# Optimization experiments

Measured on AMD Instinct MI355X. Metric: run time of the kernel, lower is better.

## Reference

```python
import jax, jax.numpy as jnp
import numpy as np

BATCH, INPUT_SIZE, STEPS = 256, 512, 256
HIDDEN = 512


def setup_inputs() -> dict:
    key = jax.random.key(0)
    ks = jax.random.split(key, 5)
    s = 1.0 / np.sqrt(HIDDEN)
    return {
        "x": jax.random.normal(ks[0], (BATCH, INPUT_SIZE, STEPS), dtype=jnp.float32),
        "weight_ih": jax.random.uniform(ks[1], (3 * HIDDEN, INPUT_SIZE), jnp.float32, -s, s),
        "weight_hh": jax.random.uniform(ks[2], (3 * HIDDEN, HIDDEN), jnp.float32, -s, s),
        "bias_ih": jax.random.uniform(ks[3], (3 * HIDDEN,), jnp.float32, -s, s),
        "bias_hh": jax.random.uniform(ks[4], (3 * HIDDEN,), jnp.float32, -s, s),
    }


def reference(x, weight_ih, weight_hh, bias_ih, bias_hh):
    # x: [B, input_size, steps]; run a GRUCell over the time axis, return final hidden.
    B = x.shape[0]
    # Precompute all input projections in one big GEMM: [steps, B, 3H]
    gi_all = jnp.einsum('bis,gi->sbg', x, weight_ih) + bias_ih

    def step(h, gi):
        gh = h @ weight_hh.T + bias_hh  # [B, 3H]
        i_r, i_z, i_n = jnp.split(gi, 3, axis=-1)
        h_r, h_z, h_n = jnp.split(gh, 3, axis=-1)
        r = jax.nn.sigmoid(i_r + h_r)
        z = jax.nn.sigmoid(i_z + h_z)
        n = jnp.tanh(i_n + r * h_n)
        h_new = (1.0 - z) * n + z * h
        return h_new, None

    h0 = jnp.zeros((B, HIDDEN), dtype=x.dtype)
    h_final, _ = jax.lax.scan(step, h0, gi_all)
    return h_final
```

## Files before the change

### kernel.cpp

```cpp
#include <hip/hip_runtime.h>
#include <stdint.h>

typedef __attribute__((ext_vector_type(8))) short bf16x8;
typedef __attribute__((ext_vector_type(4))) short s16x4;
typedef __attribute__((ext_vector_type(4))) float f32x4;

#define AS1 __attribute__((address_space(1)))
#define AS3 __attribute__((address_space(3)))

static __device__ __forceinline__ void gload_lds16(const void* g, void* l) {
  __builtin_amdgcn_global_load_lds((const AS1 unsigned int*)g,
                                   (AS3 unsigned int*)l, 16, 0, 0);
}

static __device__ __forceinline__ short f2bs(float f) {
  unsigned u = __builtin_bit_cast(unsigned, f);
  unsigned r = (u + 0x7fffu + ((u >> 16) & 1u)) >> 16;
  return (short)r;
}
static __device__ __forceinline__ float bs2f(short s) {
  unsigned u = ((unsigned)(unsigned short)s) << 16;
  return __builtin_bit_cast(float, u);
}

static __device__ __forceinline__ float sigmoid_f(float x) {
  return 1.0f / (1.0f + __expf(-x));
}
static __device__ __forceinline__ float tanh_f(float x) {
  float ax = fabsf(x);
  float e  = __expf(-2.0f * ax);
  float t  = (1.0f - e) / (1.0f + e);
  return copysignf(t, x);
}

#define BATCH 256
#define HID   512
#define STEPS 256
#define G3    1536

__global__ __launch_bounds__(256) void convert_kernel(const float* __restrict__ src,
                                                      short* __restrict__ dst, int n4) {
  int i = blockIdx.x * 256 + threadIdx.x;
  if (i < n4) {
    float4 v = *(const float4*)(src + (size_t)i * 4);
    s16x4 o;
    o[0] = f2bs(v.x); o[1] = f2bs(v.y); o[2] = f2bs(v.z); o[3] = f2bs(v.w);
    *(s16x4*)(dst + (size_t)i * 4) = o;
  }
}

__global__ __launch_bounds__(256) void transpose_kernel(const float* __restrict__ x,
                                                        short* __restrict__ xT) {
  int bx = blockIdx.x;
  int st = bx & 7, it = (bx >> 3) & 15, b = bx >> 7;
  int s0 = st * 32, i0 = it * 32;
  int tid = threadIdx.x;
  __shared__ float tile[32][33];
  int il = tid >> 3, s4 = (tid & 7) * 4;
  float4 v = *(const float4*)(x + (size_t)b * 131072 + (size_t)(i0 + il) * 256 + s0 + s4);
  tile[il][s4 + 0] = v.x; tile[il][s4 + 1] = v.y;
  tile[il][s4 + 2] = v.z; tile[il][s4 + 3] = v.w;
  __syncthreads();
  int sl = tid >> 3, iv = (tid & 7) * 4;
  s16x4 o;
  o[0] = f2bs(tile[iv + 0][sl]); o[1] = f2bs(tile[iv + 1][sl]);
  o[2] = f2bs(tile[iv + 2][sl]); o[3] = f2bs(tile[iv + 3][sl]);
  *(s16x4*)(xT + (size_t)(s0 + sl) * 131072 + (size_t)b * 512 + i0 + iv) = o;
}

__global__ __launch_bounds__(256) void phase1_kernel(const short* __restrict__ A,
                                                     const short* __restrict__ B,
                                                     const float* __restrict__ bias,
                                                     short* __restrict__ out, int M) {
  int MT = M >> 7;
  int bx = blockIdx.x;
  int mt = bx % MT, nt = bx / MT;
  int m0 = mt * 128, n0 = nt * 128;
  int tid = threadIdx.x, w = tid >> 6, lane = tid & 63;
  int lm = lane & 15, q = lane >> 4;
  int wm = w & 1, wn = w >> 1;
  __shared__ short As[128 * 32];
  __shared__ short Bs[128 * 32];
  f32x4 acc[4][4] = {};
  int srow = lane >> 2;
  int scol = (lane & 3) * 8;

  for (int kt = 0; kt < 16; ++kt) {
#pragma unroll
    for (int i2 = 0; i2 < 2; ++i2) {
      int i = w * 2 + i2;
      int row = i * 16 + srow;
      gload_lds16(A + (size_t)(m0 + row) * 512 + kt * 32 + scol, As + i * 512);
      gload_lds16(B + (size_t)(n0 + row) * 512 + kt * 32 + scol, Bs + i * 512);
    }
    __syncthreads();
    bf16x8 av[4], bv[4];
#pragma unroll
    for (int f = 0; f < 4; ++f) {
      av[f] = *(const bf16x8*)(As + (wm * 64 + f * 16 + lm) * 32 + q * 8);
      bv[f] = *(const bf16x8*)(Bs + (wn * 64 + f * 16 + lm) * 32 + q * 8);
    }
#pragma unroll
    for (int fm = 0; fm < 4; ++fm)
#pragma unroll
      for (int fn = 0; fn < 4; ++fn)
        acc[fm][fn] = __builtin_amdgcn_mfma_f32_16x16x32_bf16(av[fm], bv[fn], acc[fm][fn], 0, 0, 0);
    __syncthreads();
  }
#pragma unroll
  for (int fn = 0; fn < 4; ++fn) {
    int g = n0 + wn * 64 + fn * 16 + lm;
    float bi = bias[g];
#pragma unroll
    for (int fm = 0; fm < 4; ++fm) {
      int rb = m0 + wm * 64 + fm * 16 + q * 4;
#pragma unroll
      for (int r = 0; r < 4; ++r)
        out[(size_t)(rb + r) * G3 + g] = f2bs(acc[fm][fn][r] + bi);
    }
  }
}

__global__ __launch_bounds__(256) void scan_kernel(const short* __restrict__ gi,
                                                   const short* __restrict__ Whh,
                                                   const float* __restrict__ bias_hh,
                                                   short* __restrict__ hbuf,
                                                   unsigned* __restrict__ counters,
                                                   float* __restrict__ hmaster,
                                                   int CH, int step_base, int first) {
  int bid = blockIdx.x;
  int xcd = bid & 7, slot = bid >> 3;
  int group = xcd + 8 * (slot >> 4);
  int j = slot & 15;
  int tid = threadIdx.x;
  int w = tid >> 6, lane = tid & 63;
  int lm = lane & 15, q = lane >> 4;
  int grow = group * 16;

  __shared__ short h_lds[16 * 520];
  __shared__ float gh_lds[16][100];
  __shared__ float h_loc[512];
  __shared__ float bhh[96];

  bf16x8 Bf[2][16];
  if (w < 3) {
#pragma unroll
    for (int tau = 0; tau < 2; ++tau)
#pragma unroll
      for (int kt = 0; kt < 16; ++kt) {
        int row = w * 512 + j * 32 + tau * 16 + lm;
        Bf[tau][kt] = *(const bf16x8*)(Whh + (size_t)row * 512 + kt * 32 + q * 8);
      }
  }

  if (tid < 96) {
    int p = tid >> 5, cc = tid & 31;
    bhh[tid] = bias_hh[p * 512 + j * 32 + cc];
  }
#pragma unroll
  for (int u = 0; u < 2; ++u) {
    int idx = tid + u * 256;
    int r = idx >> 5, cc = idx & 31;
    h_loc[idx] = first ? 0.0f : hmaster[(size_t)(grow + r) * 512 + j * 32 + cc];
  }
  __syncthreads();

  int i0 = tid, i1 = tid + 256;
  const short* gp0 = gi + (size_t)(grow + (i0 >> 5)) * G3 + j * 32 + (i0 & 31);
  const short* gp1 = gi + (size_t)(grow + (i1 >> 5)) * G3 + j * 32 + (i1 & 31);
  const size_t gstride = (size_t)256 * G3;

  short pg0r = gp0[0], pg0z = gp0[512], pg0n = gp0[1024];
  short pg1r = gp1[0], pg1z = gp1[512], pg1n = gp1[1024];

  for (int t = 0; t < CH; ++t) {
    int gstep = step_base + t;
    int p = gstep & 1;
    const short* hsrc = hbuf + (size_t)p * (256 * 512) + (size_t)grow * 512;
    const short* pa = hsrc + (size_t)(tid >> 6) * 512 + (size_t)(tid & 63) * 8;

    bf16x8 t0, t1, t2, t3;
    asm volatile(
        "global_load_dwordx4 %0, %4, off sc0 sc1\n\t"
        "global_load_dwordx4 %1, %5, off sc0 sc1\n\t"
        "global_load_dwordx4 %2, %6, off sc0 sc1\n\t"
        "global_load_dwordx4 %3, %7, off sc0 sc1\n\t"
        "s_waitcnt vmcnt(0)"
        : "=&v"(t0), "=&v"(t1), "=&v"(t2), "=&v"(t3)
        : "v"(pa), "v"(pa + 2048), "v"(pa + 4096), "v"(pa + 6144)
        : "memory");

    float cg0r = bs2f(pg0r), cg0z = bs2f(pg0z), cg0n = bs2f(pg0n);
    float cg1r = bs2f(pg1r), cg1z = bs2f(pg1z), cg1n = bs2f(pg1n);
    {
      size_t o = (size_t)((t + 1 < CH) ? (t + 1) : t) * gstride;
      pg0r = gp0[o]; pg0z = gp0[o + 512]; pg0n = gp0[o + 1024];
      pg1r = gp1[o]; pg1z = gp1[o + 512]; pg1n = gp1[o + 1024];
    }

    short* ld = h_lds + (tid >> 6) * 520 + (tid & 63) * 8;
    *(bf16x8*)(ld)            = t0;
    *(bf16x8*)(ld + 4 * 520)  = t1;
    *(bf16x8*)(ld + 8 * 520)  = t2;
    *(bf16x8*)(ld + 12 * 520) = t3;
    __syncthreads();

    if (w < 3) {
      f32x4 a0 = {0.f,0.f,0.f,0.f}, a1 = {0.f,0.f,0.f,0.f};
      f32x4 a2 = {0.f,0.f,0.f,0.f}, a3 = {0.f,0.f,0.f,0.f};
#pragma unroll
      for (int kt = 0; kt < 8; ++kt) {
        bf16x8 a = *(const bf16x8*)(h_lds + lm * 520 + kt * 32 + q * 8);
        a0 = __builtin_amdgcn_mfma_f32_16x16x32_bf16(a, Bf[0][kt], a0, 0, 0, 0);
        a1 = __builtin_amdgcn_mfma_f32_16x16x32_bf16(a, Bf[1][kt], a1, 0, 0, 0);
      }
#pragma unroll
      for (int kt = 8; kt < 16; ++kt) {
        bf16x8 a = *(const bf16x8*)(h_lds + lm * 520 + kt * 32 + q * 8);
        a2 = __builtin_amdgcn_mfma_f32_16x16x32_bf16(a, Bf[0][kt], a2, 0, 0, 0);
        a3 = __builtin_amdgcn_mfma_f32_16x16x32_bf16(a, Bf[1][kt], a3, 0, 0, 0);
      }
#pragma unroll
      for (int r = 0; r < 4; ++r) {
        gh_lds[q * 4 + r][w * 32 + lm]      = a0[r] + a2[r];
        gh_lds[q * 4 + r][w * 32 + 16 + lm] = a1[r] + a3[r];
      }
    }
    __syncthreads();

    {
      int r = i0 >> 5, cc = i0 & 31;
      float hr = gh_lds[r][cc]      + bhh[cc];
      float hz = gh_lds[r][32 + cc] + bhh[32 + cc];
      float hn = gh_lds[r][64 + cc] + bhh[64 + cc];
      float rr = sigmoid_f(cg0r + hr);
      float zz = sigmoid_f(cg0z + hz);
      float nn = tanh_f(cg0n + rr * hn);
      h_loc[i0] = (1.0f - zz) * nn + zz * h_loc[i0];
    }
    {
      int r = i1 >> 5, cc = i1 & 31;
      float hr = gh_lds[r][cc]      + bhh[cc];
      float hz = gh_lds[r][32 + cc] + bhh[32 + cc];
      float hn = gh_lds[r][64 + cc] + bhh[64 + cc];
      float rr = sigmoid_f(cg1r + hr);
      float zz = sigmoid_f(cg1z + hz);
      float nn = tanh_f(cg1n + rr * hn);
      h_loc[i1] = (1.0f - zz) * nn + zz * h_loc[i1];
    }
    __syncthreads();

    if (w == 0) {
      short* hdst = hbuf + (size_t)(1 - p) * (256 * 512)
                  + (size_t)(grow + (lane >> 2)) * 512 + j * 32 + (lane & 3) * 8;
      int base = (lane >> 2) * 32 + (lane & 3) * 8;
      bf16x8 hb;
#pragma unroll
      for (int e = 0; e < 8; ++e) hb[e] = f2bs(h_loc[base + e]);
      asm volatile("global_store_dwordx4 %0, %1, off sc0 sc1\n\ts_waitcnt vmcnt(0)"
                   :: "v"(hdst), "v"(hb) : "memory");
      if (lane == 0) {
        unsigned* cp = counters + (size_t)(group * 16 + j) * 16;
        unsigned val = (unsigned)(gstep + 1);
        asm volatile("global_store_dword %0, %1, off sc0 sc1" :: "v"(cp), "v"(val) : "memory");
      }
    } else if (w == 1) {
      if (t < CH - 1 && lane < 16) {
        const unsigned* cpl = counters + (size_t)(group * 16 + lane) * 16;
        unsigned tgt = (unsigned)(gstep + 1);
        unsigned v; int it = 0;
        do {
          asm volatile("global_load_dword %0, %1, off sc0 sc1\n\ts_waitcnt vmcnt(0)"
                       : "=v"(v) : "v"(cpl) : "memory");
          if (v >= tgt) break;
          __builtin_amdgcn_s_sleep(1);
        } while (++it < (1 << 20));
      }
    }
    __syncthreads();
  }

#pragma unroll
  for (int u = 0; u < 2; ++u) {
    int idx = tid + u * 256;
    int r = idx >> 5, cc = idx & 31;
    hmaster[(size_t)(grow + r) * 512 + j * 32 + cc] = h_loc[idx];
  }
}

extern "C" void kernel_launch(void* const* d_in, const int* in_sizes, int n_in,
                              void* d_out, int out_size, void* d_ws, size_t ws_size,
                              hipStream_t stream) {
  const float* x   = (const float*)d_in[0];
  const float* Wih = (const float*)d_in[1];
  const float* Whh = (const float*)d_in[2];
  const float* bih = (const float*)d_in[3];
  const float* bhh = (const float*)d_in[4];
  float* out = (float*)d_out;
  char* ws = (char*)d_ws;

  const size_t XT_BYTES   = (size_t)256 * 256 * 512 * 2;
  const size_t W_BYTES    = (size_t)1536 * 512 * 2;
  const size_t HBUF_BYTES = (size_t)2 * 256 * 512 * 2;
  const size_t CNT_BYTES  = 16384;
  const size_t FIXED = XT_BYTES + 2 * W_BYTES + HBUF_BYTES + CNT_BYTES + 4096;

  int CH = 256;
  while (CH > 4 && FIXED + (size_t)CH * 256 * G3 * 2 > ws_size) CH >>= 1;

  size_t off = 0;
  short* gi = (short*)(ws + off);          off += (size_t)CH * 256 * G3 * 2;
  short* xT = (short*)(ws + off);          off += XT_BYTES;
  short* WihB = (short*)(ws + off);        off += W_BYTES;
  short* WhhB = (short*)(ws + off);        off += W_BYTES;
  short* hbuf = (short*)(ws + off);        off += HBUF_BYTES;
  unsigned* counters = (unsigned*)(ws + off);

  hipMemsetAsync(hbuf, 0, HBUF_BYTES + CNT_BYTES, stream);

  convert_kernel<<<768, 256, 0, stream>>>(Wih, WihB, 196608);
  convert_kernel<<<768, 256, 0, stream>>>(Whh, WhhB, 196608);
  transpose_kernel<<<32768, 256, 0, stream>>>(x, xT);

  int nch = 256 / CH;
  for (int c = 0; c < nch; ++c) {
    int M = CH * 256;
    phase1_kernel<<<(M / 128) * 12, 256, 0, stream>>>(
        xT + (size_t)c * CH * 256 * 512, WihB, bih, gi, M);
    scan_kernel<<<256, 256, 0, stream>>>(gi, WhhB, bhh, hbuf, counters, out,
                                         CH, c * CH, c == 0 ? 1 : 0);
  }
}
```

Baseline: 1.079 ms.

## Replace counter-based cross-block barrier with step-tagged hidden-state words

Each hidden-state element is now stored as a 32-bit word holding the bf16 value in the high half and the step number in the low half. Consumers poll the hidden buffer until every tag matches the expected step, then strip the tags into LDS. This removes the separate counter store/poll phase and two block-wide barriers per step. In exchange the hidden-state traffic doubles, and readers re-fetch the whole tile while spinning.

```diff
diff --git a/kernel.cpp b/kernel.cpp
--- a/kernel.cpp
+++ b/kernel.cpp
@@ -4,6 +4,7 @@
 typedef __attribute__((ext_vector_type(8))) short bf16x8;
 typedef __attribute__((ext_vector_type(4))) short s16x4;
 typedef __attribute__((ext_vector_type(4))) float f32x4;
+typedef __attribute__((ext_vector_type(4))) unsigned u32x4;
 
 #define AS1 __attribute__((address_space(1)))
 #define AS3 __attribute__((address_space(3)))
@@ -124,8 +125,7 @@
 __global__ __launch_bounds__(256) void scan_kernel(const short* __restrict__ gi,
                                                    const short* __restrict__ Whh,
                                                    const float* __restrict__ bias_hh,
-                                                   short* __restrict__ hbuf,
-                                                   unsigned* __restrict__ counters,
+                                                   unsigned* __restrict__ hbuf,
                                                    float* __restrict__ hmaster,
                                                    int CH, int step_base, int first) {
   int bid = blockIdx.x;
@@ -173,22 +173,60 @@
   short pg0r = gp0[0], pg0z = gp0[512], pg0n = gp0[1024];
   short pg1r = gp1[0], pg1z = gp1[512], pg1n = gp1[1024];
 
+  unsigned o0 = (unsigned)tid * 16u;
+  const int r0 = tid >> 7;
+  const int colb = (tid & 127) * 4;
+  short* lp = h_lds + r0 * 520 + colb;
+  unsigned* grp_base = hbuf + (size_t)group * 8192;
+
   for (int t = 0; t < CH; ++t) {
     int gstep = step_base + t;
     int p = gstep & 1;
-    const short* hsrc = hbuf + (size_t)p * (256 * 512) + (size_t)grow * 512;
-    const short* pa = hsrc + (size_t)(tid >> 6) * 512 + (size_t)(tid & 63) * 8;
-
-    bf16x8 t0, t1, t2, t3;
-    asm volatile(
-        "global_load_dwordx4 %0, %4, off sc0 sc1\n\t"
-        "global_load_dwordx4 %1, %5, off sc0 sc1\n\t"
-        "global_load_dwordx4 %2, %6, off sc0 sc1\n\t"
-        "global_load_dwordx4 %3, %7, off sc0 sc1\n\t"
-        "s_waitcnt vmcnt(0)"
-        : "=&v"(t0), "=&v"(t1), "=&v"(t2), "=&v"(t3)
-        : "v"(pa), "v"(pa + 2048), "v"(pa + 4096), "v"(pa + 6144)
-        : "memory");
+    const unsigned* src = grp_base + (size_t)p * 131072;
+    unsigned want = (unsigned)gstep;
+
+    u32x4 v0, v1, v2, v3, v4, v5, v6, v7;
+    int spin = 0;
+    for (;;) {
+      asm volatile(
+          "global_load_dwordx4 %0, %8, %16 sc0 sc1\n\t"
+          "global_load_dwordx4 %1, %9, %16 sc0 sc1\n\t"
+          "global_load_dwordx4 %2, %10, %16 sc0 sc1\n\t"
+          "global_load_dwordx4 %3, %11, %16 sc0 sc1\n\t"
+          "global_load_dwordx4 %4, %12, %16 sc0 sc1\n\t"
+          "global_load_dwordx4 %5, %13, %16 sc0 sc1\n\t"
+          "global_load_dwordx4 %6, %14, %16 sc0 sc1\n\t"
+          "global_load_dwordx4 %7, %15, %16 sc0 sc1\n\t"
+          "s_waitcnt vmcnt(0)"
+          : "=&v"(v0), "=&v"(v1), "=&v"(v2), "=&v"(v3),
+            "=&v"(v4), "=&v"(v5), "=&v"(v6), "=&v"(v7)
+          : "v"(o0), "v"(o0 + 4096u), "v"(o0 + 8192u), "v"(o0 + 12288u),
+            "v"(o0 + 16384u), "v"(o0 + 20480u), "v"(o0 + 24576u), "v"(o0 + 28672u),
+            "s"(src)
+          : "memory");
+      unsigned d;
+      d  = (v0[0] ^ want) | (v0[1] ^ want) | (v0[2] ^ want) | (v0[3] ^ want);
+      d |= (v1[0] ^ want) | (v1[1] ^ want) | (v1[2] ^ want) | (v1[3] ^ want);
+      d |= (v2[0] ^ want) | (v2[1] ^ want) | (v2[2] ^ want) | (v2[3] ^ want);
+      d |= (v3[0] ^ want) | (v3[1] ^ want) | (v3[2] ^ want) | (v3[3] ^ want);
+      d |= (v4[0] ^ want) | (v4[1] ^ want) | (v4[2] ^ want) | (v4[3] ^ want);
+      d |= (v5[0] ^ want) | (v5[1] ^ want) | (v5[2] ^ want) | (v5[3] ^ want);
+      d |= (v6[0] ^ want) | (v6[1] ^ want) | (v6[2] ^ want) | (v6[3] ^ want);
+      d |= (v7[0] ^ want) | (v7[1] ^ want) | (v7[2] ^ want) | (v7[3] ^ want);
+      if (((d & 0xffffu) == 0u) || (++spin > (1 << 16))) break;
+      __builtin_amdgcn_s_sleep(1);
+    }
+
+#define STASH(vv, c)                                                         \
+    {                                                                        \
+      s16x4 o_;                                                              \
+      o_[0] = (short)(vv[0] >> 16); o_[1] = (short)(vv[1] >> 16);            \
+      o_[2] = (short)(vv[2] >> 16); o_[3] = (short)(vv[3] >> 16);            \
+      *(s16x4*)(lp + (c) * 1040) = o_;                                       \
+    }
+    STASH(v0, 0) STASH(v1, 1) STASH(v2, 2) STASH(v3, 3)
+    STASH(v4, 4) STASH(v5, 5) STASH(v6, 6) STASH(v7, 7)
+#undef STASH
 
     float cg0r = bs2f(pg0r), cg0z = bs2f(pg0z), cg0n = bs2f(pg0n);
     float cg1r = bs2f(pg1r), cg1z = bs2f(pg1z), cg1n = bs2f(pg1n);
@@ -197,12 +235,6 @@
       pg0r = gp0[o]; pg0z = gp0[o + 512]; pg0n = gp0[o + 1024];
       pg1r = gp1[o]; pg1z = gp1[o + 512]; pg1n = gp1[o + 1024];
     }
-
-    short* ld = h_lds + (tid >> 6) * 520 + (tid & 63) * 8;
-    *(bf16x8*)(ld)            = t0;
-    *(bf16x8*)(ld + 4 * 520)  = t1;
-    *(bf16x8*)(ld + 8 * 520)  = t2;
-    *(bf16x8*)(ld + 12 * 520) = t3;
     __syncthreads();
 
     if (w < 3) {
@@ -228,6 +260,8 @@
     }
     __syncthreads();
 
+    unsigned tagp = (unsigned)(gstep + 1);
+    unsigned* dstb = grp_base + (size_t)(1 - p) * 131072;
     {
       int r = i0 >> 5, cc = i0 & 31;
       float hr = gh_lds[r][cc]      + bhh[cc];
@@ -236,7 +270,11 @@
       float rr = sigmoid_f(cg0r + hr);
       float zz = sigmoid_f(cg0z + hz);
       float nn = tanh_f(cg0n + rr * hn);
-      h_loc[i0] = (1.0f - zz) * nn + zz * h_loc[i0];
+      float hv = (1.0f - zz) * nn + zz * h_loc[i0];
+      h_loc[i0] = hv;
+      unsigned val = (((unsigned)(unsigned short)f2bs(hv)) << 16) | tagp;
+      unsigned* dp = dstb + r * 512 + j * 32 + cc;
+      asm volatile("global_store_dword %0, %1, off sc0 sc1" :: "v"(dp), "v"(val) : "memory");
     }
     {
       int r = i1 >> 5, cc = i1 & 31;
@@ -246,38 +284,12 @@
       float rr = sigmoid_f(cg1r + hr);
       float zz = sigmoid_f(cg1z + hz);
       float nn = tanh_f(cg1n + rr * hn);
-      h_loc[i1] = (1.0f - zz) * nn + zz * h_loc[i1];
-    }
-    __syncthreads();
-
-    if (w == 0) {
-      short* hdst = hbuf + (size_t)(1 - p) * (256 * 512)
-                  + (size_t)(grow + (lane >> 2)) * 512 + j * 32 + (lane & 3) * 8;
-      int base = (lane >> 2) * 32 + (lane & 3) * 8;
-      bf16x8 hb;
-#pragma unroll
-      for (int e = 0; e < 8; ++e) hb[e] = f2bs(h_loc[base + e]);
-      asm volatile("global_store_dwordx4 %0, %1, off sc0 sc1\n\ts_waitcnt vmcnt(0)"
-                   :: "v"(hdst), "v"(hb) : "memory");
-      if (lane == 0) {
-        unsigned* cp = counters + (size_t)(group * 16 + j) * 16;
-        unsigned val = (unsigned)(gstep + 1);
-        asm volatile("global_store_dword %0, %1, off sc0 sc1" :: "v"(cp), "v"(val) : "memory");
-      }
-    } else if (w == 1) {
-      if (t < CH - 1 && lane < 16) {
-        const unsigned* cpl = counters + (size_t)(group * 16 + lane) * 16;
-        unsigned tgt = (unsigned)(gstep + 1);
-        unsigned v; int it = 0;
-        do {
-          asm volatile("global_load_dword %0, %1, off sc0 sc1\n\ts_waitcnt vmcnt(0)"
-                       : "=v"(v) : "v"(cpl) : "memory");
-          if (v >= tgt) break;
-          __builtin_amdgcn_s_sleep(1);
-        } while (++it < (1 << 20));
-      }
-    }
-    __syncthreads();
+      float hv = (1.0f - zz) * nn + zz * h_loc[i1];
+      h_loc[i1] = hv;
+      unsigned val = (((unsigned)(unsigned short)f2bs(hv)) << 16) | tagp;
+      unsigned* dp = dstb + r * 512 + j * 32 + cc;
+      asm volatile("global_store_dword %0, %1, off sc0 sc1" :: "v"(dp), "v"(val) : "memory");
+    }
   }
 
 #pragma unroll
@@ -301,9 +313,8 @@
 
   const size_t XT_BYTES   = (size_t)256 * 256 * 512 * 2;
   const size_t W_BYTES    = (size_t)1536 * 512 * 2;
-  const size_t HBUF_BYTES = (size_t)2 * 256 * 512 * 2;
-  const size_t CNT_BYTES  = 16384;
-  const size_t FIXED = XT_BYTES + 2 * W_BYTES + HBUF_BYTES + CNT_BYTES + 4096;
+  const size_t HBUF_BYTES = (size_t)2 * 256 * 512 * 4;
+  const size_t FIXED = XT_BYTES + 2 * W_BYTES + HBUF_BYTES + 4096;
 
   int CH = 256;
   while (CH > 4 && FIXED + (size_t)CH * 256 * G3 * 2 > ws_size) CH >>= 1;
@@ -313,10 +324,9 @@
   short* xT = (short*)(ws + off);          off += XT_BYTES;
   short* WihB = (short*)(ws + off);        off += W_BYTES;
   short* WhhB = (short*)(ws + off);        off += W_BYTES;
-  short* hbuf = (short*)(ws + off);        off += HBUF_BYTES;
-  unsigned* counters = (unsigned*)(ws + off);
-
-  hipMemsetAsync(hbuf, 0, HBUF_BYTES + CNT_BYTES, stream);
+  unsigned* hbuf = (unsigned*)(ws + off);
+
+  hipMemsetAsync(hbuf, 0, HBUF_BYTES, stream);
 
   convert_kernel<<<768, 256, 0, stream>>>(Wih, WihB, 196608);
   convert_kernel<<<768, 256, 0, stream>>>(Whh, WhhB, 196608);
@@ -327,7 +337,7 @@
     int M = CH * 256;
     phase1_kernel<<<(M / 128) * 12, 256, 0, stream>>>(
         xT + (size_t)c * CH * 256 * 512, WihB, bih, gi, M);
-    scan_kernel<<<256, 256, 0, stream>>>(gi, WhhB, bhh, hbuf, counters, out,
+    scan_kernel<<<256, 256, 0, stream>>>(gi, WhhB, bhh, hbuf, out,
                                          CH, c * CH, c == 0 ? 1 : 0);
   }
 }
```

After: 888.6 us. 1.21x faster.
